# Performance work log

Hardware: AMD Instinct MI355X
Metric: run time of the kernel (lower is better)

## Reference

```python
import jax, jax.numpy as jnp
import numpy as np

EPS_RMS = 1e-6   # assumed eps for utils.rms
EPS_LN = 1e-5    # matches F.layer_norm eps in LayerNorm


def rmsnorm(z):
    # utils.rms: normalize to unit RMS over the channel dim
    return z * jax.lax.rsqrt(jnp.mean(jnp.square(z), axis=-1, keepdims=True) + EPS_RMS)


def layernorm(x, w):
    mu = jnp.mean(x, axis=-1, keepdims=True)
    var = jnp.var(x, axis=-1, keepdims=True)
    return (x - mu) * jax.lax.rsqrt(var + EPS_LN) * w


def polar_orthogonal(W):
    # utils.fast_polar_decomposition: orthogonal factor of polar decomposition
    U, _, Vh = jnp.linalg.svd(W, full_matrices=False)
    return U @ Vh


def pscan2(q, P1, P2, identity):
    # Hillis-Steele inclusive parallel scan over the time axis with combine
    # scan(left, right) = rms(left @ P1^T + right @ P2^T); positions with no
    # left operand at a level keep their current value (identity pads the shift).
    B, T, C = q.shape
    d = 1
    while d < T:
        left = jnp.concatenate(
            [jnp.broadcast_to(identity, (B, d, C)), q[:, : T - d]], axis=1)
        z = rmsnorm(jnp.einsum('btc,dc->btd', left, P1)
                    + jnp.einsum('btc,dc->btd', q, P2))
        upd = (jnp.arange(T) >= d)[None, :, None]
        q = jnp.where(upd, z, q)
        d *= 2
    return q


def setup_inputs() -> dict:
    key = jax.random.key(0)
    ks = jax.random.split(key, 9)
    B, T, C = 4, 4096, 512
    inv = 1.0 / np.sqrt(C)
    return {
        'x': jax.random.normal(ks[0], (B, T, C), jnp.float32),
        'ln1_w': jnp.ones((C,), jnp.float32),
        'Wq': jax.random.normal(ks[1], (C, C), jnp.float32) * inv,
        'Wv': jax.random.normal(ks[2], (C, C), jnp.float32) * inv,
        'Wo': jax.random.normal(ks[3], (C, C), jnp.float32) * inv,
        'identity': jax.random.uniform(ks[4], (C,), jnp.float32),
        'Wp1': jax.random.normal(ks[5], (C, C), jnp.float32),
        'Wp2': jax.random.normal(ks[6], (C, C), jnp.float32),
        'ln2_w': jnp.ones((C,), jnp.float32),
        'Wfc': jax.random.normal(ks[7], (4 * C, C), jnp.float32) * inv,
        'Wpr': jax.random.normal(ks[8], (C, 4 * C), jnp.float32) * (1.0 / np.sqrt(4 * C)),
    }


def reference(x, ln1_w, Wq, Wv, Wo, identity, Wp1, Wp2, ln2_w, Wfc, Wpr):
    # SSM branch (dropout = 0 in eval)
    h = layernorm(x, ln1_w)
    q = h @ Wq.T
    v = h @ Wv.T
    P1 = polar_orthogonal(Wp1)
    P2 = polar_orthogonal(Wp2)
    q = pscan2(q, P1, P2, identity)
    x = x + (q * v) @ Wo.T
    # MLP branch
    h2 = layernorm(x, ln2_w)
    h2 = jax.nn.gelu(h2 @ Wfc.T, approximate=False)  # torch nn.GELU() is exact erf
    x = x + h2 @ Wpr.T
    return x
```

## Files before the change

### kernel.cpp

```cpp
#include <hip/hip_runtime.h>
#include <hip/hip_bf16.h>

typedef __hip_bfloat16 bf16;
typedef __attribute__((ext_vector_type(8))) short short8;
typedef __attribute__((ext_vector_type(4))) short short4v;
typedef __attribute__((ext_vector_type(4))) float f32x4;

#define DEVINL static __device__ __forceinline__

DEVINL float b2f(bf16 x) { return __bfloat162float(x); }
DEVINL bf16 f2b(float x) { return __float2bfloat16(x); }
DEVINL float sb2f(short s) { return b2f(__builtin_bit_cast(bf16, s)); }
DEVINL short f2sb(float x) { return __builtin_bit_cast(short, f2b(x)); }

DEVINL void gload16(const void* g, void* l) {
  __builtin_amdgcn_global_load_lds(
      (const __attribute__((address_space(1))) void*)g,
      (__attribute__((address_space(3))) void*)l, 16, 0, 0);
}

DEVINL float wave_sum(float v) {
#pragma unroll
  for (int o = 32; o > 0; o >>= 1) v += __shfl_down(v, o, 64);
  return v;
}

DEVINL float wave_allsum(float v) {
#pragma unroll
  for (int o = 32; o > 0; o >>= 1) v += __shfl_xor(v, o, 64);
  return v;
}

DEVINL float gelu_exact(float v) {
  const float z = v * 0.70710678118654752f;
  const float az = fabsf(z);
  const float t = 1.0f / (1.0f + 0.3275911f * az);
  float p = 1.061405429f;
  p = p * t - 1.453152027f;
  p = p * t + 1.421413741f;
  p = p * t - 0.284496736f;
  p = p * t + 0.254829592f;
  const float e = __expf(-z * z);
  const float erf_az = 1.0f - p * t * e;
  const float er = (z < 0.f) ? -erf_az : erf_az;
  return 0.5f * v * (1.0f + er);
}

#define BARRIER()                             \
  do {                                        \
    __asm__ __volatile__("" ::: "memory");    \
    __builtin_amdgcn_s_barrier();             \
    __asm__ __volatile__("" ::: "memory");    \
  } while (0)
#define WAIT_LGKM0() __asm__ __volatile__("s_waitcnt lgkmcnt(0)" ::: "memory")
#define WAIT_VM(n) __asm__ __volatile__("s_waitcnt vmcnt(" #n ")" ::: "memory")

template <int MODE, bool SPLIT, int BM>
__global__ __launch_bounds__(256) void gemm_nt(
    const bf16* __restrict__ A0, const bf16* __restrict__ A1,
    const bf16* __restrict__ B0, const bf16* __restrict__ B1,
    int K, int lda, int ldb, long bsA, long bsB, long bsC,
    float alpha, float beta, float* __restrict__ Xf,
    bf16* __restrict__ Whi, bf16* __restrict__ Wlo,
    bf16* __restrict__ Thi, bf16* __restrict__ Tlo) {
  constexpr int BK = 64;
  constexpr int MT = BM / 32;
  constexpr int NLOAD = BM * BK / 2048;
  extern __shared__ char smem[];
  bf16* AsH = (bf16*)smem;
  bf16* BsH = AsH + BM * BK;
  bf16* AsL = BsH + BM * BK;
  bf16* BsL = AsL + BM * BK;

  const int t = threadIdx.x;
  const int lane = t & 63, w = t >> 6;
  const long bz = blockIdx.z;
  const bf16* Ab0 = A0 + bz * bsA;
  const bf16* Bb0 = B0 + bz * bsB;
  const bf16* Ab1 = SPLIT ? (A1 + bz * bsA) : nullptr;
  const bf16* Bb1 = SPLIT ? (B1 + bz * bsB) : nullptr;

  const int row0 = blockIdx.x * BM, col0 = blockIdx.y * BM;
  const int wm = (w >> 1) * (BM / 2), wn = (w & 1) * (BM / 2);
  const int jj = lane >> 4, r16 = lane & 15;

  f32x4 acc[MT][MT] = {};

  for (int k0 = 0; k0 < K; k0 += BK) {
    __syncthreads();
#pragma unroll
    for (int s = 0; s < NLOAD; ++s) {
      const int L = s * 256 + t;
      const int cj = L / BM, m = L % BM;
      const long ga = (long)(row0 + m) * lda + (k0 + cj * 8);
      const long gb = (long)(col0 + m) * ldb + (k0 + cj * 8);
      gload16(Ab0 + ga, AsH + L * 8);
      gload16(Bb0 + gb, BsH + L * 8);
      if (SPLIT) {
        gload16(Ab1 + ga, AsL + L * 8);
        gload16(Bb1 + gb, BsL + L * 8);
      }
    }
    __syncthreads();

#pragma unroll
    for (int kk = 0; kk < BK / 32; ++kk) {
      short8 a[MT], b[MT], al[MT], bl[MT];
#pragma unroll
      for (int mt = 0; mt < MT; ++mt) {
        const int o = (kk * 4 + jj) * BM * 8 + (wm + mt * 16 + r16) * 8;
        a[mt] = *(const short8*)(AsH + o);
        if (SPLIT) al[mt] = *(const short8*)(AsL + o);
      }
#pragma unroll
      for (int nt = 0; nt < MT; ++nt) {
        const int o = (kk * 4 + jj) * BM * 8 + (wn + nt * 16 + r16) * 8;
        b[nt] = *(const short8*)(BsH + o);
        if (SPLIT) bl[nt] = *(const short8*)(BsL + o);
      }
#pragma unroll
      for (int mt = 0; mt < MT; ++mt)
#pragma unroll
        for (int nt = 0; nt < MT; ++nt) {
          acc[mt][nt] = __builtin_amdgcn_mfma_f32_16x16x32_bf16(a[mt], b[nt], acc[mt][nt], 0, 0, 0);
          if (SPLIT) {
            acc[mt][nt] = __builtin_amdgcn_mfma_f32_16x16x32_bf16(a[mt], bl[nt], acc[mt][nt], 0, 0, 0);
            acc[mt][nt] = __builtin_amdgcn_mfma_f32_16x16x32_bf16(al[mt], b[nt], acc[mt][nt], 0, 0, 0);
          }
        }
    }
  }

#pragma unroll
  for (int mt = 0; mt < MT; ++mt)
#pragma unroll
    for (int nt = 0; nt < MT; ++nt)
#pragma unroll
      for (int r = 0; r < 4; ++r) {
        const int row = row0 + wm + mt * 16 + jj * 4 + r;
        const int col = col0 + wn + nt * 16 + r16;
        const float v = acc[mt][nt][r];
        if (MODE == 3) {
          const long i = bz * bsC + (long)row * 512 + col;
          const bf16 h = f2b(v);
          Whi[i] = h;
          Wlo[i] = f2b(v - b2f(h));
        } else if (MODE == 4) {
          const long i = bz * bsC + (long)row * 512 + col;
          const float nv = alpha * Xf[i] + beta * v;
          Xf[i] = nv;
          const bf16 h = f2b(nv);
          const bf16 l = f2b(nv - b2f(h));
          Whi[i] = h; Wlo[i] = l;
          const long it2 = bz * bsC + (long)col * 512 + row;
          Thi[it2] = h; Tlo[it2] = l;
        }
      }
}

DEVINL void loadA4(const bf16* p, short8 (&dst)[4][2]) {
#pragma unroll
  for (int mf = 0; mf < 4; ++mf)
#pragma unroll
    for (int kk = 0; kk < 2; ++kk)
      dst[mf][kk] = *(const short8*)(p + kk * 4096 + mf * 128);
}
DEVINL void loadB2(const bf16* p, short8 (&dst)[2][2]) {
#pragma unroll
  for (int nf = 0; nf < 2; ++nf)
#pragma unroll
    for (int kk = 0; kk < 2; ++kk)
      dst[nf][kk] = *(const short8*)(p + kk * 4096 + nf * 128);
}
template <int QM, int QN>
DEVINL void mfma16(const short8 (&af)[4][2], const short8 (&bb)[2][2],
                   f32x4 (&acc)[8][4]) {
  __builtin_amdgcn_s_setprio(1);
#pragma unroll
  for (int mf = 0; mf < 4; ++mf)
#pragma unroll
    for (int nf = 0; nf < 2; ++nf)
#pragma unroll
      for (int kk = 0; kk < 2; ++kk)
        acc[QM * 4 + mf][QN * 2 + nf] = __builtin_amdgcn_mfma_f32_16x16x32_bf16(
            af[mf][kk], bb[nf][kk], acc[QM * 4 + mf][QN * 2 + nf], 0, 0, 0);
  __builtin_amdgcn_s_setprio(0);
}
template <int QM>
DEVINL void mfma16h(const short8 (&af)[4][2], const short8 (&bb)[2][2],
                    f32x4 (&acc)[8][2]) {
  __builtin_amdgcn_s_setprio(1);
#pragma unroll
  for (int mf = 0; mf < 4; ++mf)
#pragma unroll
    for (int nf = 0; nf < 2; ++nf)
#pragma unroll
      for (int kk = 0; kk < 2; ++kk)
        acc[QM * 4 + mf][nf] = __builtin_amdgcn_mfma_f32_16x16x32_bf16(
            af[mf][kk], bb[nf][kk], acc[QM * 4 + mf][nf], 0, 0, 0);
  __builtin_amdgcn_s_setprio(0);
}

template <int MODE, int BN>
__global__ __launch_bounds__(512, 2) void gemm256(
    const bf16* __restrict__ A, const bf16* __restrict__ B, int K, int lda,
    int ldb, bf16* __restrict__ outb, int ldo, const float* __restrict__ resf,
    float* __restrict__ outf) {
  extern __shared__ char smem[];
  const int t = threadIdx.x;
  const int lane = t & 63;
  const int w = t >> 6, wr = w >> 2, wc = w & 3;
  const int jj = lane >> 4, r16 = lane & 15;
  const int sm = t & 127, cj = t >> 7;

  int bx, by;
  {
    const int gx = gridDim.x;
    const int nwg = gx * gridDim.y;
    int lin = blockIdx.y * gx + blockIdx.x;
    lin = (lin & 7) * (nwg >> 3) + (lin >> 3);
    bx = lin % gx;
    by = lin / gx;
  }
  const int row0 = bx * 256;
  const int col0 = by * BN;

  const int aBase = (jj * 128 + wr * 64 + r16) * 8;
  const int bBase = (jj * 128 + wc * 32 + r16) * 8;

  if constexpr (BN == 256) {
    auto slotp = [&](int buf, int mat, int half) -> bf16* {
      return (bf16*)(smem + (((buf << 2) | (mat << 1) | half) << 14));
    };
    auto stageA = [&](int buf, int half, int kt) {
      bf16* dst = slotp(buf, 0, half) + t * 8;
      const long ga = (long)(row0 + half * 128 + sm) * lda + kt * 64 + cj * 8;
      gload16(A + ga, dst);
      gload16(A + ga + 32, dst + 4096);
    };
    auto stageB = [&](int buf, int half, int kt) {
      bf16* dst = slotp(buf, 1, half) + t * 8;
      const long gb = (long)(col0 + half * 128 + sm) * ldb + kt * 64 + cj * 8;
      gload16(B + gb, dst);
      gload16(B + gb + 32, dst + 4096);
    };

    f32x4 acc[8][4] = {};
    const int nit = K >> 7;

    stageA(0, 0, 0); stageB(0, 0, 0);
    stageB(0, 1, 0);
    stageA(0, 1, 0);
    stageA(1, 0, 1); stageB(1, 0, 1);
    stageB(1, 1, 1);
    WAIT_VM(8);
    BARRIER();

    for (int it = 0; it < nit; ++it) {
      const int k1 = 2 * it + 1, k2 = 2 * it + 2, k3 = 2 * it + 3;
      const bool more = (it + 1 < nit);
      short8 af[4][2], b0[2][2], b1[2][2];
      loadA4(slotp(0, 0, 0) + aBase, af);
      loadB2(slotp(0, 1, 0) + bBase, b0);
      stageA(1, 1, k1);
      BARRIER(); WAIT_LGKM0();
      mfma16<0, 0>(af, b0, acc);
      loadB2(slotp(0, 1, 1) + bBase, b1);
      WAIT_VM(8);
      BARRIER(); WAIT_LGKM0();
      mfma16<0, 1>(af, b1, acc);
      loadA4(slotp(0, 0, 1) + aBase, af);
      if (more) { stageA(0, 0, k2); stageB(0, 0, k2); }
      BARRIER(); WAIT_LGKM0();
      mfma16<1, 1>(af, b1, acc);
      if (more) { stageB(0, 1, k2); WAIT_VM(8); } else { WAIT_VM(0); }
      BARRIER();
      mfma16<1, 0>(af, b0, acc);
      loadA4(slotp(1, 0, 0) + aBase, af);
      loadB2(slotp(1, 1, 0) + bBase, b0);
      if (more) stageA(0, 1, k2);
      BARRIER(); WAIT_LGKM0();
      mfma16<0, 0>(af, b0, acc);
      loadB2(slotp(1, 1, 1) + bBase, b1);
      WAIT_VM(8);
      BARRIER(); WAIT_LGKM0();
      mfma16<0, 1>(af, b1, acc);
      loadA4(slotp(1, 0, 1) + aBase, af);
      if (more) { stageA(1, 0, k3); stageB(1, 0, k3); }
      BARRIER(); WAIT_LGKM0();
      mfma16<1, 1>(af, b1, acc);
      if (more) { stageB(1, 1, k3); WAIT_VM(8); }
      BARRIER();
      mfma16<1, 0>(af, b0, acc);
    }

    if constexpr (MODE == 2) {
#pragma unroll
      for (int q = 0; q < 8; ++q)
#pragma unroll
        for (int n = 0; n < 4; ++n)
#pragma unroll
          for (int r = 0; r < 4; ++r) {
            const int row = row0 + (q >> 2) * 128 + wr * 64 + (q & 3) * 16 + jj * 4 + r;
            const int col = col0 + (n >> 1) * 128 + wc * 32 + (n & 1) * 16 + r16;
            const long i = (long)row * ldo + col;
            outf[i] = resf[i] + acc[q][n][r];
          }
      return;
    } else {
      __syncthreads();
      bf16* Cs = (bf16*)smem;
#pragma unroll
      for (int q = 0; q < 8; ++q)
#pragma unroll
        for (int n = 0; n < 4; ++n)
#pragma unroll
          for (int r = 0; r < 4; ++r) {
            const int row = (q >> 2) * 128 + wr * 64 + (q & 3) * 16 + jj * 4 + r;
            const int col = (n >> 1) * 128 + wc * 32 + (n & 1) * 16 + r16;
            float v = acc[q][n][r];
            if (MODE == 1) v = gelu_exact(v);
            Cs[row * 256 + col] = f2b(v);
          }
      __syncthreads();
#pragma unroll
      for (int i = 0; i < 16; ++i) {
        const int rr = i * 16 + (t >> 5);
        const int cc = (t & 31) * 8;
        *(short8*)(outb + (long)(row0 + rr) * ldo + (col0 + cc)) =
            *(const short8*)(Cs + rr * 256 + cc);
      }
    }
  } else {
    auto slotp3 = [&](int buf, int slot) -> bf16* {
      return (bf16*)(smem + ((buf * 3 + slot) << 14));
    };
    auto stage3A = [&](int buf, int half, int kt) {
      bf16* dst = slotp3(buf, half) + t * 8;
      const long ga = (long)(row0 + half * 128 + sm) * lda + kt * 64 + cj * 8;
      gload16(A + ga, dst);
      gload16(A + ga + 32, dst + 4096);
    };
    auto stage3B = [&](int buf, int kt) {
      bf16* dst = slotp3(buf, 2) + t * 8;
      const long gb = (long)(col0 + sm) * ldb + kt * 64 + cj * 8;
      gload16(B + gb, dst);
      gload16(B + gb + 32, dst + 4096);
    };

    f32x4 acc[8][2] = {};
    const int nt = K >> 6;

    stage3A(0, 0, 0); stage3A(0, 1, 0); stage3B(0, 0);
    stage3A(1, 0, 1); stage3A(1, 1, 1); stage3B(1, 1);
    WAIT_VM(6);
    BARRIER();

    int cb = 0;
    for (int tk = 0; tk < nt; ++tk) {
      int sb = cb + 2; if (sb >= 3) sb -= 3;
      const bool more = (tk + 2 < nt);
      short8 af[4][2], bb2[2][2];
      bf16* sA0 = slotp3(cb, 0);
      bf16* sA1 = slotp3(cb, 1);
      bf16* sB = slotp3(cb, 2);
      loadA4(sA0 + aBase, af);
      loadB2(sB + bBase, bb2);
      if (more) { stage3A(sb, 0, tk + 2); stage3B(sb, tk + 2); }
      BARRIER(); WAIT_LGKM0();
      mfma16h<0>(af, bb2, acc);
      loadA4(sA1 + aBase, af);
      if (more) stage3A(sb, 1, tk + 2);
      if (more) { WAIT_VM(6); } else { WAIT_VM(0); }
      BARRIER(); WAIT_LGKM0();
      mfma16h<1>(af, bb2, acc);
      cb = (cb + 1 == 3) ? 0 : cb + 1;
    }

#pragma unroll
    for (int q = 0; q < 8; ++q)
#pragma unroll
      for (int n = 0; n < 2; ++n)
#pragma unroll
        for (int r = 0; r < 4; ++r) {
          const int row = row0 + (q >> 2) * 128 + wr * 64 + (q & 3) * 16 + jj * 4 + r;
          const int col = col0 + wc * 32 + n * 16 + r16;
          const long i = (long)row * ldo + col;
          outf[i] = resf[i] + acc[q][n][r];
        }
  }
}

__global__ __launch_bounds__(256) void fnorm(const float* __restrict__ W1,
                                             const float* __restrict__ W2,
                                             float* __restrict__ sigsq) {
  const int b = blockIdx.x >> 8;
  const float4 v = *(const float4*)((b ? W2 : W1) +
                                    (((long)(blockIdx.x & 255) * 256 + threadIdx.x) << 2));
  float s = v.x * v.x + v.y * v.y + v.z * v.z + v.w * v.w;
  s = wave_sum(s);
  if ((threadIdx.x & 63) == 0) atomicAdd(&sigsq[b], s);
}

__global__ __launch_bounds__(256) void scale_init(
    const float* __restrict__ W1, const float* __restrict__ W2,
    const float* __restrict__ sigsq, float* __restrict__ Xf,
    bf16* __restrict__ Xhi, bf16* __restrict__ Xlo,
    bf16* __restrict__ Thi, bf16* __restrict__ Tlo) {
  const long idx = (long)blockIdx.x * 256 + threadIdx.x;
  const int b = (int)(idx >> 18);
  const int i = (int)(idx & 262143);
  const float s = rsqrtf(sigsq[b]);
  const float val = (b ? W2[i] : W1[i]) * s;
  const long o = ((long)b << 18) + i;
  Xf[o] = val;
  const bf16 h = f2b(val);
  const bf16 l = f2b(val - b2f(h));
  Xhi[o] = h; Xlo[o] = l;
  const int r = i >> 9, c = i & 511;
  const long ot = ((long)b << 18) + (long)c * 512 + r;
  Thi[ot] = h; Tlo[ot] = l;
}

__global__ __launch_bounds__(256) void convert_weights(
    const float* __restrict__ Wq, const float* __restrict__ Wv,
    const float* __restrict__ Wo, const float* __restrict__ Wfc,
    const float* __restrict__ Wpr, bf16* __restrict__ Wqvb,
    bf16* __restrict__ Wob, bf16* __restrict__ Wfcb, bf16* __restrict__ Wprb) {
  const long e = ((long)blockIdx.x * 256 + threadIdx.x) << 2;
  const float* src; bf16* dst; long off;
  if (e < 262144)       { src = Wq;  dst = Wqvb;          off = e; }
  else if (e < 524288)  { src = Wv;  dst = Wqvb + 262144; off = e - 262144; }
  else if (e < 786432)  { src = Wo;  dst = Wob;           off = e - 524288; }
  else if (e < 1835008) { src = Wfc; dst = Wfcb;          off = e - 786432; }
  else                  { src = Wpr; dst = Wprb;          off = e - 1835008; }
  const float4 v = *(const float4*)(src + off);
  short4v o4;
  o4[0] = f2sb(v.x); o4[1] = f2sb(v.y); o4[2] = f2sb(v.z); o4[3] = f2sb(v.w);
  *(short4v*)(dst + off) = o4;
}

__global__ __launch_bounds__(256) void ln_rows(const float* __restrict__ x,
                                               const float* __restrict__ w,
                                               bf16* __restrict__ out) {
  const int row = (blockIdx.x << 2) + (threadIdx.x >> 6);
  const int lane = threadIdx.x & 63;
  const float* xr = x + (long)row * 512 + lane * 8;
  const float4 a = *(const float4*)xr;
  const float4 b = *(const float4*)(xr + 4);
  float v[8] = {a.x, a.y, a.z, a.w, b.x, b.y, b.z, b.w};
  float s1 = 0.f, s2 = 0.f;
#pragma unroll
  for (int i = 0; i < 8; ++i) { s1 += v[i]; s2 += v[i] * v[i]; }
  s1 = wave_allsum(s1);
  s2 = wave_allsum(s2);
  const float mean = s1 * (1.0f / 512.0f);
  const float var = s2 * (1.0f / 512.0f) - mean * mean;
  const float inv = rsqrtf(var + 1e-5f);
  const float4 w1 = *(const float4*)(w + lane * 8);
  const float4 w2 = *(const float4*)(w + lane * 8 + 4);
  const float wv[8] = {w1.x, w1.y, w1.z, w1.w, w2.x, w2.y, w2.z, w2.w};
  short8 o8;
#pragma unroll
  for (int i = 0; i < 8; ++i) o8[i] = f2sb((v[i] - mean) * inv * wv[i]);
  *(short8*)(out + (long)row * 512 + lane * 8) = o8;
}

__global__ __launch_bounds__(256) void pscan_combine2(const bf16* __restrict__ Y,
                                                      bf16* __restrict__ QV, int d) {
  const int span = 4096 - d;
  const int wid = (blockIdx.x << 2) + (threadIdx.x >> 6);
  const int lane = threadIdx.x & 63;
  const int b = wid / span;
  const int tt = d + (wid - b * span);
  const long row2 = (long)b * 4096 + tt;
  const long row1 = row2 - d;
  const short8 a8 = *(const short8*)(Y + row1 * 1024 + lane * 8);
  const short8 b8 = *(const short8*)(Y + row2 * 1024 + 512 + lane * 8);
  float s[8]; float ss = 0.f;
#pragma unroll
  for (int i = 0; i < 8; ++i) {
    const float v = sb2f(a8[i]) + sb2f(b8[i]);
    s[i] = v; ss += v * v;
  }
  ss = wave_allsum(ss);
  const float inv = rsqrtf(ss * (1.0f / 512.0f) + 1e-6f);
  short8 o8;
#pragma unroll
  for (int i = 0; i < 8; ++i) o8[i] = f2sb(s[i] * inv);
  *(short8*)(QV + row2 * 1024 + lane * 8) = o8;
}

__global__ __launch_bounds__(256) void qv_mul(const bf16* __restrict__ QV,
                                              bf16* __restrict__ u) {
  const long base = ((long)blockIdx.x * 256 + threadIdx.x) << 3;
  const long row = base >> 9;
  const int c = (int)(base & 511);
  const short8 q8 = *(const short8*)(QV + row * 1024 + c);
  const short8 v8 = *(const short8*)(QV + row * 1024 + 512 + c);
  short8 o8;
#pragma unroll
  for (int i = 0; i < 8; ++i) o8[i] = f2sb(sb2f(q8[i]) * sb2f(v8[i]));
  *(short8*)(u + row * 512 + c) = o8;
}

extern "C" void kernel_launch(void* const* d_in, const int* in_sizes, int n_in,
                              void* d_out, int out_size, void* d_ws, size_t ws_size,
                              hipStream_t stream) {
  (void)in_sizes; (void)n_in; (void)out_size; (void)ws_size;
  const float* x    = (const float*)d_in[0];
  const float* ln1w = (const float*)d_in[1];
  const float* Wq   = (const float*)d_in[2];
  const float* Wv   = (const float*)d_in[3];
  const float* Wo   = (const float*)d_in[4];
  const float* Wp1  = (const float*)d_in[6];
  const float* Wp2  = (const float*)d_in[7];
  const float* ln2w = (const float*)d_in[8];
  const float* Wfc  = (const float*)d_in[9];
  const float* Wpr  = (const float*)d_in[10];
  float* out = (float*)d_out;

  const long M = 16384;
  char* ws = (char*)d_ws;
  size_t off = 0;
  auto alloc = [&](size_t bytes) -> void* {
    void* p = ws + off;
    off += (bytes + 255) & ~(size_t)255;
    return p;
  };
  bf16* YZ   = (bf16*)alloc(M * 1024 * 2);
  bf16* QV   = (bf16*)alloc(M * 1024 * 2);
  bf16* hb   = (bf16*)alloc(M * 512 * 2);
  bf16* Wqvb = (bf16*)alloc(1024 * 512 * 2);
  bf16* Wob  = (bf16*)alloc(512 * 512 * 2);
  bf16* Wfcb = (bf16*)alloc(2048 * 512 * 2);
  bf16* Wprb = (bf16*)alloc(512 * 2048 * 2);
  float* Xf  = (float*)alloc(2 * 262144 * 4);
  bf16* Xhi  = (bf16*)alloc(2 * 262144 * 2);
  bf16* Xlo  = (bf16*)alloc(2 * 262144 * 2);
  bf16* XtAh = (bf16*)alloc(2 * 262144 * 2);
  bf16* XtAl = (bf16*)alloc(2 * 262144 * 2);
  bf16* XtBh = (bf16*)alloc(2 * 262144 * 2);
  bf16* XtBl = (bf16*)alloc(2 * 262144 * 2);
  bf16* Ghi  = (bf16*)alloc(2 * 262144 * 2);
  bf16* Glo  = (bf16*)alloc(2 * 262144 * 2);
  float* sig = (float*)alloc(256);
  bf16* Y  = YZ;
  bf16* h3 = YZ;

  const auto Z0 = nullptr;

  hipMemsetAsync(sig, 0, 2 * sizeof(float), stream);
  fnorm<<<512, 256, 0, stream>>>(Wp1, Wp2, sig);
  scale_init<<<2048, 256, 0, stream>>>(Wp1, Wp2, sig, Xf, Xhi, Xlo, XtAh, XtAl);

  bf16 *tch = XtAh, *tcl = XtAl, *tnh = XtBh, *tnl = XtBl;
  const long Sz = 262144;
  for (int i = 0; i < 20; ++i) {
    const bool pol = (i >= 16);
    const float ac = pol ? 1.5f : 2.0f;
    const float bc = pol ? -0.5f : -1.0f;
    dim3 g(8, 8, 2);
    gemm_nt<3, true, 64><<<g, 256, 32768, stream>>>(
        Xhi, Xlo, Xhi, Xlo, 512, 512, 512, Sz, Sz, Sz,
        0.f, 0.f, Z0, Ghi, Glo, Z0, Z0);
    gemm_nt<4, true, 64><<<g, 256, 32768, stream>>>(
        Ghi, Glo, tch, tcl, 512, 512, 512, Sz, Sz, Sz,
        ac, bc, Xf, Xhi, Xlo, tnh, tnl);
    bf16* sw;
    sw = tch; tch = tnh; tnh = sw;
    sw = tcl; tcl = tnl; tnl = sw;
  }

  convert_weights<<<2816, 256, 0, stream>>>(Wq, Wv, Wo, Wfc, Wpr, Wqvb, Wob, Wfcb, Wprb);

  ln_rows<<<4096, 256, 0, stream>>>(x, ln1w, hb);
  gemm256<0, 256><<<dim3(64, 4), 512, 131072, stream>>>(
      hb, Wqvb, 512, 512, 512, QV, 1024, Z0, Z0);

  for (int d = 1; d < 4096; d <<= 1) {
    gemm256<0, 256><<<dim3(64, 4), 512, 131072, stream>>>(
        QV, Xhi, 512, 1024, 512, Y, 1024, Z0, Z0);
    pscan_combine2<<<4096 - d, 256, 0, stream>>>(Y, QV, d);
  }

  qv_mul<<<4096, 256, 0, stream>>>(QV, hb);
  gemm256<2, 128><<<dim3(64, 4), 512, 147456, stream>>>(
      hb, Wob, 512, 512, 512, Z0, 512, x, out);

  ln_rows<<<4096, 256, 0, stream>>>(out, ln2w, hb);
  gemm256<1, 256><<<dim3(64, 8), 512, 131072, stream>>>(
      hb, Wfcb, 512, 512, 512, h3, 2048, Z0, Z0);
  gemm256<2, 128><<<dim3(64, 4), 512, 147456, stream>>>(
      h3, Wprb, 2048, 2048, 2048, Z0, 512, out, out);
}
```

Before: 1.466 ms.

## Fuse pscan shifted operands into one K=1024 GEMM and skip finished rows

Each pscan level now runs a single GEMM whose A operand concatenates the d-shifted left row with the current row along K (K=1024), against a repacked [P1|P2] weight. This removes the separate add of two halves of a 1024-wide output. The grid covers only row tiles from d rounded down to 256, so already-final prefix rows are skipped at later levels. The BN=128 path gains a bf16 LDS-staged epilogue and reorders its prefetch issue. The costs are a 2x deeper K per tile, clamped addressing for shifted rows, and the swizzled block mapping being dropped for all GEMMs.

```diff
diff --git a/kernel.cpp b/kernel.cpp
--- a/kernel.cpp
+++ b/kernel.cpp
@@ -201,11 +201,11 @@
   __builtin_amdgcn_s_setprio(0);
 }
 
-template <int MODE, int BN>
+template <int MODE, int BN, bool PSCAN>
 __global__ __launch_bounds__(512, 2) void gemm256(
     const bf16* __restrict__ A, const bf16* __restrict__ B, int K, int lda,
     int ldb, bf16* __restrict__ outb, int ldo, const float* __restrict__ resf,
-    float* __restrict__ outf) {
+    float* __restrict__ outf, int d, int start, int nyb) {
   extern __shared__ char smem[];
   const int t = threadIdx.x;
   const int lane = t & 63;
@@ -213,17 +213,16 @@
   const int jj = lane >> 4, r16 = lane & 15;
   const int sm = t & 127, cj = t >> 7;
 
-  int bx, by;
-  {
-    const int gx = gridDim.x;
-    const int nwg = gx * gridDim.y;
-    int lin = blockIdx.y * gx + blockIdx.x;
-    lin = (lin & 7) * (nwg >> 3) + (lin >> 3);
-    bx = lin % gx;
-    by = lin / gx;
+  int row0, batch0 = 0;
+  if (PSCAN) {
+    const int b = blockIdx.x / nyb;
+    const int ty = blockIdx.x - b * nyb;
+    batch0 = b * 4096;
+    row0 = batch0 + start + ty * 256;
+  } else {
+    row0 = blockIdx.x * 256;
   }
-  const int row0 = bx * 256;
-  const int col0 = by * BN;
+  const int col0 = blockIdx.y * BN;
 
   const int aBase = (jj * 128 + wr * 64 + r16) * 8;
   const int bBase = (jj * 128 + wc * 32 + r16) * 8;
@@ -337,7 +336,19 @@
     };
     auto stage3A = [&](int buf, int half, int kt) {
       bf16* dst = slotp3(buf, half) + t * 8;
-      const long ga = (long)(row0 + half * 128 + sm) * lda + kt * 64 + cj * 8;
+      long ga;
+      if (PSCAN) {
+        const int rr = row0 + half * 128 + sm;
+        if (kt < 8) {
+          int rs = rr - d;
+          if (rs < batch0) rs = batch0;
+          ga = (long)rs * 1024 + kt * 64 + cj * 8;
+        } else {
+          ga = (long)rr * 1024 + (kt - 8) * 64 + cj * 8;
+        }
+      } else {
+        ga = (long)(row0 + half * 128 + sm) * lda + kt * 64 + cj * 8;
+      }
       gload16(A + ga, dst);
       gload16(A + ga + 32, dst + 4096);
     };
@@ -366,29 +377,64 @@
       bf16* sB = slotp3(cb, 2);
       loadA4(sA0 + aBase, af);
       loadB2(sB + bBase, bb2);
-      if (more) { stage3A(sb, 0, tk + 2); stage3B(sb, tk + 2); }
       BARRIER(); WAIT_LGKM0();
       mfma16h<0>(af, bb2, acc);
       loadA4(sA1 + aBase, af);
-      if (more) stage3A(sb, 1, tk + 2);
-      if (more) { WAIT_VM(6); } else { WAIT_VM(0); }
+      if (more) {
+        stage3A(sb, 0, tk + 2); stage3A(sb, 1, tk + 2); stage3B(sb, tk + 2);
+        WAIT_VM(6);
+      } else {
+        WAIT_VM(0);
+      }
       BARRIER(); WAIT_LGKM0();
       mfma16h<1>(af, bb2, acc);
       cb = (cb + 1 == 3) ? 0 : cb + 1;
     }
 
-#pragma unroll
-    for (int q = 0; q < 8; ++q)
-#pragma unroll
-      for (int n = 0; n < 2; ++n)
-#pragma unroll
-        for (int r = 0; r < 4; ++r) {
-          const int row = row0 + (q >> 2) * 128 + wr * 64 + (q & 3) * 16 + jj * 4 + r;
-          const int col = col0 + wc * 32 + n * 16 + r16;
-          const long i = (long)row * ldo + col;
-          outf[i] = resf[i] + acc[q][n][r];
-        }
+    if constexpr (MODE == 2) {
+#pragma unroll
+      for (int q = 0; q < 8; ++q)
+#pragma unroll
+        for (int n = 0; n < 2; ++n)
+#pragma unroll
+          for (int r = 0; r < 4; ++r) {
+            const int row = row0 + (q >> 2) * 128 + wr * 64 + (q & 3) * 16 + jj * 4 + r;
+            const int col = col0 + wc * 32 + n * 16 + r16;
+            const long i = (long)row * ldo + col;
+            outf[i] = resf[i] + acc[q][n][r];
+          }
+    } else {
+      __syncthreads();
+      bf16* Cs = (bf16*)smem;
+#pragma unroll
+      for (int q = 0; q < 8; ++q)
+#pragma unroll
+        for (int n = 0; n < 2; ++n)
+#pragma unroll
+          for (int r = 0; r < 4; ++r) {
+            const int row = (q >> 2) * 128 + wr * 64 + (q & 3) * 16 + jj * 4 + r;
+            const int col = wc * 32 + n * 16 + r16;
+            Cs[row * 128 + col] = f2b(acc[q][n][r]);
+          }
+      __syncthreads();
+#pragma unroll
+      for (int i = 0; i < 8; ++i) {
+        const int rr = i * 32 + (t >> 4);
+        const int cc = (t & 15) * 8;
+        *(short8*)(outb + (long)(row0 + rr) * ldo + (col0 + cc)) =
+            *(const short8*)(Cs + rr * 128 + cc);
+      }
+    }
   }
+}
+
+__global__ __launch_bounds__(256) void repack_pcat(const bf16* __restrict__ Xhi,
+                                                   bf16* __restrict__ Pcat) {
+  const int e = (blockIdx.x * 256 + threadIdx.x) << 3;
+  const int c = e >> 10, k = e & 1023;
+  const bf16* src = (k < 512) ? (Xhi + (long)c * 512 + k)
+                              : (Xhi + 262144 + (long)c * 512 + (k - 512));
+  *(short8*)(Pcat + e) = *(const short8*)src;
 }
 
 __global__ __launch_bounds__(256) void fnorm(const float* __restrict__ W1,
@@ -466,21 +512,19 @@
   *(short8*)(out + (long)row * 512 + lane * 8) = o8;
 }
 
-__global__ __launch_bounds__(256) void pscan_combine2(const bf16* __restrict__ Y,
-                                                      bf16* __restrict__ QV, int d) {
+__global__ __launch_bounds__(256) void pscan_combine(const bf16* __restrict__ S,
+                                                     bf16* __restrict__ QV, int d) {
   const int span = 4096 - d;
   const int wid = (blockIdx.x << 2) + (threadIdx.x >> 6);
   const int lane = threadIdx.x & 63;
   const int b = wid / span;
   const int tt = d + (wid - b * span);
-  const long row2 = (long)b * 4096 + tt;
-  const long row1 = row2 - d;
-  const short8 a8 = *(const short8*)(Y + row1 * 1024 + lane * 8);
-  const short8 b8 = *(const short8*)(Y + row2 * 1024 + 512 + lane * 8);
+  const long rowQ = (long)b * 4096 + tt;
+  const short8 s8 = *(const short8*)(S + rowQ * 512 + lane * 8);
   float s[8]; float ss = 0.f;
 #pragma unroll
   for (int i = 0; i < 8; ++i) {
-    const float v = sb2f(a8[i]) + sb2f(b8[i]);
+    const float v = sb2f(s8[i]);
     s[i] = v; ss += v * v;
   }
   ss = wave_allsum(ss);
@@ -488,7 +532,7 @@
   short8 o8;
 #pragma unroll
   for (int i = 0; i < 8; ++i) o8[i] = f2sb(s[i] * inv);
-  *(short8*)(QV + row2 * 1024 + lane * 8) = o8;
+  *(short8*)(QV + rowQ * 1024 + lane * 8) = o8;
 }
 
 __global__ __launch_bounds__(256) void qv_mul(const bf16* __restrict__ QV,
@@ -544,8 +588,9 @@
   bf16* XtBl = (bf16*)alloc(2 * 262144 * 2);
   bf16* Ghi  = (bf16*)alloc(2 * 262144 * 2);
   bf16* Glo  = (bf16*)alloc(2 * 262144 * 2);
+  bf16* Pcat = (bf16*)alloc(512 * 1024 * 2);
   float* sig = (float*)alloc(256);
-  bf16* Y  = YZ;
+  bf16* S  = YZ;
   bf16* h3 = YZ;
 
   const auto Z0 = nullptr;
@@ -571,26 +616,29 @@
     sw = tch; tch = tnh; tnh = sw;
     sw = tcl; tcl = tnl; tnl = sw;
   }
+  repack_pcat<<<256, 256, 0, stream>>>(Xhi, Pcat);
 
   convert_weights<<<2816, 256, 0, stream>>>(Wq, Wv, Wo, Wfc, Wpr, Wqvb, Wob, Wfcb, Wprb);
 
   ln_rows<<<4096, 256, 0, stream>>>(x, ln1w, hb);
-  gemm256<0, 256><<<dim3(64, 4), 512, 131072, stream>>>(
-      hb, Wqvb, 512, 512, 512, QV, 1024, Z0, Z0);
+  gemm256<0, 256, false><<<dim3(64, 4), 512, 131072, stream>>>(
+      hb, Wqvb, 512, 512, 512, QV, 1024, Z0, Z0, 0, 0, 0);
 
   for (int d = 1; d < 4096; d <<= 1) {
-    gemm256<0, 256><<<dim3(64, 4), 512, 131072, stream>>>(
-        QV, Xhi, 512, 1024, 512, Y, 1024, Z0, Z0);
-    pscan_combine2<<<4096 - d, 256, 0, stream>>>(Y, QV, d);
+    const int start = d & ~255;
+    const int nyb = (4096 - start) >> 8;
+    gemm256<0, 128, true><<<dim3(4 * nyb, 4), 512, 147456, stream>>>(
+        QV, Pcat, 1024, 1024, 1024, S, 512, Z0, Z0, d, start, nyb);
+    pscan_combine<<<4096 - d, 256, 0, stream>>>(S, QV, d);
   }
 
   qv_mul<<<4096, 256, 0, stream>>>(QV, hb);
-  gemm256<2, 128><<<dim3(64, 4), 512, 147456, stream>>>(
-      hb, Wob, 512, 512, 512, Z0, 512, x, out);
+  gemm256<2, 128, false><<<dim3(64, 4), 512, 147456, stream>>>(
+      hb, Wob, 512, 512, 512, Z0, 512, x, out, 0, 0, 0);
 
   ln_rows<<<4096, 256, 0, stream>>>(out, ln2w, hb);
-  gemm256<1, 256><<<dim3(64, 8), 512, 131072, stream>>>(
-      hb, Wfcb, 512, 512, 512, h3, 2048, Z0, Z0);
-  gemm256<2, 128><<<dim3(64, 4), 512, 147456, stream>>>(
-      h3, Wprb, 2048, 2048, 2048, Z0, 512, out, out);
-}
+  gemm256<1, 256, false><<<dim3(64, 8), 512, 131072, stream>>>(
+      hb, Wfcb, 512, 512, 512, h3, 2048, Z0, Z0, 0, 0, 0);
+  gemm256<2, 128, false><<<dim3(64, 4), 512, 147456, stream>>>(
+      h3, Wprb, 2048, 2048, 2048, Z0, 512, out, out, 0, 0, 0);
+}
```

Measured after the change: 1.498 ms. +2.2%, slower.

## Fuse parallel-scan GEMM with RMS-norm combine into one kernel per level

Applied to the files above, without the earlier changes.

Replaces the per-level pair of a GEMM (q against both polar factors into a 1024-wide Y) plus a separate combine kernel with a single kernel. It computes [q_shifted, q] @ [P1;P2]^T over K=1024, RMS-normalises in registers/LDS, and writes the new q directly, ping-ponging between two buffers. It also repacks P1/P2 into a concatenated matrix, removes the block-swizzle from gemm256, and moves all prefetch issues of gemm256 after the first MFMA half. The goal is to avoid the Y round-trip through memory and one launch per level. The tradeoff is a 64-row tile with only 256 blocks at one block per CU, each re-reading the full 1 MB weight.

```diff
diff --git a/kernel.cpp b/kernel.cpp
--- a/kernel.cpp
+++ b/kernel.cpp
@@ -213,17 +213,8 @@
   const int jj = lane >> 4, r16 = lane & 15;
   const int sm = t & 127, cj = t >> 7;
 
-  int bx, by;
-  {
-    const int gx = gridDim.x;
-    const int nwg = gx * gridDim.y;
-    int lin = blockIdx.y * gx + blockIdx.x;
-    lin = (lin & 7) * (nwg >> 3) + (lin >> 3);
-    bx = lin % gx;
-    by = lin / gx;
-  }
-  const int row0 = bx * 256;
-  const int col0 = by * BN;
+  const int row0 = blockIdx.x * 256;
+  const int col0 = blockIdx.y * BN;
 
   const int aBase = (jj * 128 + wr * 64 + r16) * 8;
   const int bBase = (jj * 128 + wc * 32 + r16) * 8;
@@ -366,12 +357,15 @@
       bf16* sB = slotp3(cb, 2);
       loadA4(sA0 + aBase, af);
       loadB2(sB + bBase, bb2);
-      if (more) { stage3A(sb, 0, tk + 2); stage3B(sb, tk + 2); }
       BARRIER(); WAIT_LGKM0();
       mfma16h<0>(af, bb2, acc);
       loadA4(sA1 + aBase, af);
-      if (more) stage3A(sb, 1, tk + 2);
-      if (more) { WAIT_VM(6); } else { WAIT_VM(0); }
+      if (more) {
+        stage3A(sb, 0, tk + 2); stage3A(sb, 1, tk + 2); stage3B(sb, tk + 2);
+        WAIT_VM(6);
+      } else {
+        WAIT_VM(0);
+      }
       BARRIER(); WAIT_LGKM0();
       mfma16h<1>(af, bb2, acc);
       cb = (cb + 1 == 3) ? 0 : cb + 1;
@@ -389,6 +383,144 @@
           outf[i] = resf[i] + acc[q][n][r];
         }
   }
+}
+
+__global__ __launch_bounds__(512, 1) void pscan_fused(
+    const bf16* __restrict__ Qsrc, int ldq, bf16* __restrict__ Qdst,
+    const bf16* __restrict__ Pcat, int d) {
+  extern __shared__ char smem[];
+  __shared__ float sums[64][4];
+  const int t = threadIdx.x;
+  const int lane = t & 63;
+  const int w = t >> 6, wr = w >> 2, wc = w & 3;
+  const int jj = lane >> 4, r16 = lane & 15;
+
+  const int b = blockIdx.x >> 6;
+  const int ty = blockIdx.x & 63;
+  const int batch0 = b * 4096;
+  const int row0 = batch0 + ty * 64;
+
+  auto Asp = [&](int buf) -> bf16* { return (bf16*)smem + buf * 4096; };
+  auto Bsp = [&](int buf) -> bf16* { return (bf16*)(smem + 16384) + buf * 32768; };
+
+  bf16* Cs = (bf16*)smem;
+
+  if (row0 - batch0 + 63 >= d) {
+    const int am = t & 63, acj = t >> 6;
+    auto stage = [&](int kt, int buf) {
+      {
+        long ga;
+        const int rr = row0 + am;
+        if (kt < 8) {
+          int rs = rr - d;
+          if (rs < batch0) rs = batch0;
+          ga = (long)rs * ldq + kt * 64 + acj * 8;
+        } else {
+          ga = (long)rr * ldq + (kt - 8) * 64 + acj * 8;
+        }
+        gload16(Qsrc + ga, Asp(buf) + t * 8);
+      }
+      bf16* bs = Bsp(buf);
+#pragma unroll
+      for (int s = 0; s < 8; ++s)
+        gload16(Pcat + (long)t * 1024 + kt * 64 + s * 8, bs + (s * 512 + t) * 8);
+    };
+
+    f32x4 acc[2][8] = {};
+    stage(0, 0);
+    WAIT_VM(0);
+    BARRIER();
+
+    int cur = 0;
+    for (int kt = 0; kt < 16; ++kt) {
+      if (kt < 15) stage(kt + 1, cur ^ 1);
+      const bf16* as = Asp(cur);
+      const bf16* bs = Bsp(cur);
+#pragma unroll
+      for (int kk = 0; kk < 2; ++kk) {
+        short8 a[2], bb[8];
+#pragma unroll
+        for (int mt = 0; mt < 2; ++mt)
+          a[mt] = *(const short8*)(as + ((kk * 4 + jj) * 64 + wr * 32 + mt * 16 + r16) * 8);
+#pragma unroll
+        for (int nt = 0; nt < 8; ++nt)
+          bb[nt] = *(const short8*)(bs + ((kk * 4 + jj) * 512 + wc * 128 + nt * 16 + r16) * 8);
+#pragma unroll
+        for (int mt = 0; mt < 2; ++mt)
+#pragma unroll
+          for (int nt = 0; nt < 8; ++nt)
+            acc[mt][nt] = __builtin_amdgcn_mfma_f32_16x16x32_bf16(
+                a[mt], bb[nt], acc[mt][nt], 0, 0, 0);
+      }
+      if (kt < 15) WAIT_VM(0);
+      WAIT_LGKM0();
+      BARRIER();
+      cur ^= 1;
+    }
+
+    float part[2][4];
+#pragma unroll
+    for (int mt = 0; mt < 2; ++mt)
+#pragma unroll
+      for (int r = 0; r < 4; ++r) {
+        float s = 0.f;
+#pragma unroll
+        for (int nt = 0; nt < 8; ++nt) {
+          const float v = acc[mt][nt][r];
+          s += v * v;
+        }
+        part[mt][r] = s;
+      }
+#pragma unroll
+    for (int off = 1; off < 16; off <<= 1)
+#pragma unroll
+      for (int mt = 0; mt < 2; ++mt)
+#pragma unroll
+        for (int r = 0; r < 4; ++r)
+          part[mt][r] += __shfl_xor(part[mt][r], off, 64);
+    if (r16 == 0) {
+#pragma unroll
+      for (int mt = 0; mt < 2; ++mt)
+#pragma unroll
+        for (int r = 0; r < 4; ++r)
+          sums[wr * 32 + mt * 16 + jj * 4 + r][wc] = part[mt][r];
+    }
+    __syncthreads();
+#pragma unroll
+    for (int mt = 0; mt < 2; ++mt)
+#pragma unroll
+      for (int r = 0; r < 4; ++r) {
+        const int rl = wr * 32 + mt * 16 + jj * 4 + r;
+        const float tot = sums[rl][0] + sums[rl][1] + sums[rl][2] + sums[rl][3];
+        const float inv = rsqrtf(tot * (1.0f / 512.0f) + 1e-6f);
+#pragma unroll
+        for (int nt = 0; nt < 8; ++nt)
+          Cs[rl * 512 + wc * 128 + nt * 16 + r16] = f2b(acc[mt][nt][r] * inv);
+      }
+    __syncthreads();
+  }
+
+#pragma unroll
+  for (int s = 0; s < 8; ++s) {
+    const int j = s * 512 + t;
+    const int rl = j >> 6, c8 = (j & 63) * 8;
+    const int trel = row0 + rl - batch0;
+    short8 v8;
+    if (trel >= d)
+      v8 = *(const short8*)(Cs + rl * 512 + c8);
+    else
+      v8 = *(const short8*)(Qsrc + (long)(row0 + rl) * ldq + c8);
+    *(short8*)(Qdst + (long)(row0 + rl) * 512 + c8) = v8;
+  }
+}
+
+__global__ __launch_bounds__(256) void repack_pcat(const bf16* __restrict__ Xhi,
+                                                   bf16* __restrict__ Pcat) {
+  const int e = (blockIdx.x * 256 + threadIdx.x) << 3;
+  const int c = e >> 10, k = e & 1023;
+  const bf16* src = (k < 512) ? (Xhi + (long)c * 512 + k)
+                              : (Xhi + 262144 + (long)c * 512 + (k - 512));
+  *(short8*)(Pcat + e) = *(const short8*)src;
 }
 
 __global__ __launch_bounds__(256) void fnorm(const float* __restrict__ W1,
@@ -466,37 +598,13 @@
   *(short8*)(out + (long)row * 512 + lane * 8) = o8;
 }
 
-__global__ __launch_bounds__(256) void pscan_combine2(const bf16* __restrict__ Y,
-                                                      bf16* __restrict__ QV, int d) {
-  const int span = 4096 - d;
-  const int wid = (blockIdx.x << 2) + (threadIdx.x >> 6);
-  const int lane = threadIdx.x & 63;
-  const int b = wid / span;
-  const int tt = d + (wid - b * span);
-  const long row2 = (long)b * 4096 + tt;
-  const long row1 = row2 - d;
-  const short8 a8 = *(const short8*)(Y + row1 * 1024 + lane * 8);
-  const short8 b8 = *(const short8*)(Y + row2 * 1024 + 512 + lane * 8);
-  float s[8]; float ss = 0.f;
-#pragma unroll
-  for (int i = 0; i < 8; ++i) {
-    const float v = sb2f(a8[i]) + sb2f(b8[i]);
-    s[i] = v; ss += v * v;
-  }
-  ss = wave_allsum(ss);
-  const float inv = rsqrtf(ss * (1.0f / 512.0f) + 1e-6f);
-  short8 o8;
-#pragma unroll
-  for (int i = 0; i < 8; ++i) o8[i] = f2sb(s[i] * inv);
-  *(short8*)(QV + row2 * 1024 + lane * 8) = o8;
-}
-
-__global__ __launch_bounds__(256) void qv_mul(const bf16* __restrict__ QV,
+__global__ __launch_bounds__(256) void qv_mul(const bf16* __restrict__ Q,
+                                              const bf16* __restrict__ QV,
                                               bf16* __restrict__ u) {
   const long base = ((long)blockIdx.x * 256 + threadIdx.x) << 3;
   const long row = base >> 9;
   const int c = (int)(base & 511);
-  const short8 q8 = *(const short8*)(QV + row * 1024 + c);
+  const short8 q8 = *(const short8*)(Q + row * 512 + c);
   const short8 v8 = *(const short8*)(QV + row * 1024 + 512 + c);
   short8 o8;
 #pragma unroll
@@ -544,8 +652,10 @@
   bf16* XtBl = (bf16*)alloc(2 * 262144 * 2);
   bf16* Ghi  = (bf16*)alloc(2 * 262144 * 2);
   bf16* Glo  = (bf16*)alloc(2 * 262144 * 2);
+  bf16* Pcat = (bf16*)alloc(512 * 1024 * 2);
   float* sig = (float*)alloc(256);
-  bf16* Y  = YZ;
+  bf16* Qa = YZ;
+  bf16* Qb = YZ + 8388608;
   bf16* h3 = YZ;
 
   const auto Z0 = nullptr;
@@ -571,6 +681,7 @@
     sw = tch; tch = tnh; tnh = sw;
     sw = tcl; tcl = tnl; tnl = sw;
   }
+  repack_pcat<<<256, 256, 0, stream>>>(Xhi, Pcat);
 
   convert_weights<<<2816, 256, 0, stream>>>(Wq, Wv, Wo, Wfc, Wpr, Wqvb, Wob, Wfcb, Wprb);
 
@@ -578,13 +689,19 @@
   gemm256<0, 256><<<dim3(64, 4), 512, 131072, stream>>>(
       hb, Wqvb, 512, 512, 512, QV, 1024, Z0, Z0);
 
-  for (int d = 1; d < 4096; d <<= 1) {
-    gemm256<0, 256><<<dim3(64, 4), 512, 131072, stream>>>(
-        QV, Xhi, 512, 1024, 512, Y, 1024, Z0, Z0);
-    pscan_combine2<<<4096 - d, 256, 0, stream>>>(Y, QV, d);
+  {
+    const bf16* qsrc = QV;
+    int ldq = 1024;
+    bf16* qdst = Qa;
+    for (int d = 1; d < 4096; d <<= 1) {
+      pscan_fused<<<256, 512, 147456, stream>>>(qsrc, ldq, qdst, Pcat, d);
+      qsrc = qdst;
+      ldq = 512;
+      qdst = (qdst == Qa) ? Qb : Qa;
+    }
+    qv_mul<<<4096, 256, 0, stream>>>(qsrc, QV, hb);
   }
 
-  qv_mul<<<4096, 256, 0, stream>>>(QV, hb);
   gemm256<2, 128><<<dim3(64, 4), 512, 147456, stream>>>(
       hb, Wob, 512, 512, 512, Z0, 512, x, out);
 
```

Measured after the change: 1.667 ms. 1.14x slower.

## Pipeline Newton-Schulz split-bf16 GEMM with triple-buffered async LDS staging

Applied to the files above, without the earlier changes.

Replaces the generic single-buffered gemm_nt used in the 20 polar-decomposition iterations with a specialised gemm_ns. It has fixed K=512, triple-buffered LDS, and prefetches two tiles ahead via global_load_lds, so loads overlap the MFMA work on hi/lo splits. It also removes the XCD-style block remapping in gemm256 and moves the prefetch issue in gemm256 after the first MFMA half, which changes memory locality and overlap. The cost is three times the LDS per block (96KB), which may reduce occupancy.

```diff
diff --git a/kernel.cpp b/kernel.cpp
--- a/kernel.cpp
+++ b/kernel.cpp
@@ -55,86 +55,109 @@
 #define WAIT_LGKM0() __asm__ __volatile__("s_waitcnt lgkmcnt(0)" ::: "memory")
 #define WAIT_VM(n) __asm__ __volatile__("s_waitcnt vmcnt(" #n ")" ::: "memory")
 
-template <int MODE, bool SPLIT, int BM>
-__global__ __launch_bounds__(256) void gemm_nt(
+template <int MODE>
+__global__ __launch_bounds__(256) void gemm_ns(
     const bf16* __restrict__ A0, const bf16* __restrict__ A1,
     const bf16* __restrict__ B0, const bf16* __restrict__ B1,
-    int K, int lda, int ldb, long bsA, long bsB, long bsC,
+    long bsA, long bsB, long bsC,
     float alpha, float beta, float* __restrict__ Xf,
     bf16* __restrict__ Whi, bf16* __restrict__ Wlo,
     bf16* __restrict__ Thi, bf16* __restrict__ Tlo) {
-  constexpr int BK = 64;
-  constexpr int MT = BM / 32;
-  constexpr int NLOAD = BM * BK / 2048;
   extern __shared__ char smem[];
-  bf16* AsH = (bf16*)smem;
-  bf16* BsH = AsH + BM * BK;
-  bf16* AsL = BsH + BM * BK;
-  bf16* BsL = AsL + BM * BK;
-
   const int t = threadIdx.x;
   const int lane = t & 63, w = t >> 6;
   const long bz = blockIdx.z;
   const bf16* Ab0 = A0 + bz * bsA;
   const bf16* Bb0 = B0 + bz * bsB;
-  const bf16* Ab1 = SPLIT ? (A1 + bz * bsA) : nullptr;
-  const bf16* Bb1 = SPLIT ? (B1 + bz * bsB) : nullptr;
-
-  const int row0 = blockIdx.x * BM, col0 = blockIdx.y * BM;
-  const int wm = (w >> 1) * (BM / 2), wn = (w & 1) * (BM / 2);
+  const bf16* Ab1 = A1 + bz * bsA;
+  const bf16* Bb1 = B1 + bz * bsB;
+  const int row0 = blockIdx.x * 64, col0 = blockIdx.y * 64;
+  const int wm = (w >> 1) * 32, wn = (w & 1) * 32;
   const int jj = lane >> 4, r16 = lane & 15;
 
-  f32x4 acc[MT][MT] = {};
-
-  for (int k0 = 0; k0 < K; k0 += BK) {
-    __syncthreads();
-#pragma unroll
-    for (int s = 0; s < NLOAD; ++s) {
+  auto buf = [&](int b, int arr) -> bf16* {
+    return (bf16*)(smem + b * 32768 + arr * 8192);
+  };
+  auto stage = [&](int bi, int kt) {
+#pragma unroll
+    for (int s = 0; s < 2; ++s) {
       const int L = s * 256 + t;
-      const int cj = L / BM, m = L % BM;
-      const long ga = (long)(row0 + m) * lda + (k0 + cj * 8);
-      const long gb = (long)(col0 + m) * ldb + (k0 + cj * 8);
-      gload16(Ab0 + ga, AsH + L * 8);
-      gload16(Bb0 + gb, BsH + L * 8);
-      if (SPLIT) {
-        gload16(Ab1 + ga, AsL + L * 8);
-        gload16(Bb1 + gb, BsL + L * 8);
+      const int cj = L >> 6, m = L & 63;
+      const long ga = (long)(row0 + m) * 512 + kt * 64 + cj * 8;
+      const long gb = (long)(col0 + m) * 512 + kt * 64 + cj * 8;
+      gload16(Ab0 + ga, buf(bi, 0) + L * 8);
+      gload16(Bb0 + gb, buf(bi, 1) + L * 8);
+      gload16(Ab1 + ga, buf(bi, 2) + L * 8);
+      gload16(Bb1 + gb, buf(bi, 3) + L * 8);
+    }
+  };
+
+  f32x4 acc[2][2] = {};
+
+  stage(0, 0); stage(1, 1);
+  WAIT_VM(8);
+  BARRIER();
+
+  for (int tk = 0; tk < 8; ++tk) {
+    const int cb = tk % 3;
+    const int sb = (tk + 2) % 3;
+    bf16* ah = buf(cb, 0); bf16* bh = buf(cb, 1);
+    bf16* alp = buf(cb, 2); bf16* blp = buf(cb, 3);
+    short8 a[2], b[2], al[2], bl[2];
+#pragma unroll
+    for (int mt = 0; mt < 2; ++mt) {
+      const int o = (jj * 64 + wm + mt * 16 + r16) * 8;
+      a[mt] = *(const short8*)(ah + o);
+      al[mt] = *(const short8*)(alp + o);
+    }
+#pragma unroll
+    for (int nt = 0; nt < 2; ++nt) {
+      const int o = (jj * 64 + wn + nt * 16 + r16) * 8;
+      b[nt] = *(const short8*)(bh + o);
+      bl[nt] = *(const short8*)(blp + o);
+    }
+    BARRIER(); WAIT_LGKM0();
+#pragma unroll
+    for (int mt = 0; mt < 2; ++mt)
+#pragma unroll
+      for (int nt = 0; nt < 2; ++nt) {
+        acc[mt][nt] = __builtin_amdgcn_mfma_f32_16x16x32_bf16(a[mt], b[nt], acc[mt][nt], 0, 0, 0);
+        acc[mt][nt] = __builtin_amdgcn_mfma_f32_16x16x32_bf16(a[mt], bl[nt], acc[mt][nt], 0, 0, 0);
+        acc[mt][nt] = __builtin_amdgcn_mfma_f32_16x16x32_bf16(al[mt], b[nt], acc[mt][nt], 0, 0, 0);
       }
-    }
-    __syncthreads();
-
-#pragma unroll
-    for (int kk = 0; kk < BK / 32; ++kk) {
-      short8 a[MT], b[MT], al[MT], bl[MT];
-#pragma unroll
-      for (int mt = 0; mt < MT; ++mt) {
-        const int o = (kk * 4 + jj) * BM * 8 + (wm + mt * 16 + r16) * 8;
-        a[mt] = *(const short8*)(AsH + o);
-        if (SPLIT) al[mt] = *(const short8*)(AsL + o);
+#pragma unroll
+    for (int mt = 0; mt < 2; ++mt) {
+      const int o = ((4 + jj) * 64 + wm + mt * 16 + r16) * 8;
+      a[mt] = *(const short8*)(ah + o);
+      al[mt] = *(const short8*)(alp + o);
+    }
+#pragma unroll
+    for (int nt = 0; nt < 2; ++nt) {
+      const int o = ((4 + jj) * 64 + wn + nt * 16 + r16) * 8;
+      b[nt] = *(const short8*)(bh + o);
+      bl[nt] = *(const short8*)(blp + o);
+    }
+    if (tk + 2 < 8) {
+      stage(sb, tk + 2);
+      WAIT_VM(8);
+    } else if (tk + 1 < 8) {
+      WAIT_VM(0);
+    }
+    BARRIER(); WAIT_LGKM0();
+#pragma unroll
+    for (int mt = 0; mt < 2; ++mt)
+#pragma unroll
+      for (int nt = 0; nt < 2; ++nt) {
+        acc[mt][nt] = __builtin_amdgcn_mfma_f32_16x16x32_bf16(a[mt], b[nt], acc[mt][nt], 0, 0, 0);
+        acc[mt][nt] = __builtin_amdgcn_mfma_f32_16x16x32_bf16(a[mt], bl[nt], acc[mt][nt], 0, 0, 0);
+        acc[mt][nt] = __builtin_amdgcn_mfma_f32_16x16x32_bf16(al[mt], b[nt], acc[mt][nt], 0, 0, 0);
       }
-#pragma unroll
-      for (int nt = 0; nt < MT; ++nt) {
-        const int o = (kk * 4 + jj) * BM * 8 + (wn + nt * 16 + r16) * 8;
-        b[nt] = *(const short8*)(BsH + o);
-        if (SPLIT) bl[nt] = *(const short8*)(BsL + o);
-      }
-#pragma unroll
-      for (int mt = 0; mt < MT; ++mt)
-#pragma unroll
-        for (int nt = 0; nt < MT; ++nt) {
-          acc[mt][nt] = __builtin_amdgcn_mfma_f32_16x16x32_bf16(a[mt], b[nt], acc[mt][nt], 0, 0, 0);
-          if (SPLIT) {
-            acc[mt][nt] = __builtin_amdgcn_mfma_f32_16x16x32_bf16(a[mt], bl[nt], acc[mt][nt], 0, 0, 0);
-            acc[mt][nt] = __builtin_amdgcn_mfma_f32_16x16x32_bf16(al[mt], b[nt], acc[mt][nt], 0, 0, 0);
-          }
-        }
-    }
   }
 
 #pragma unroll
-  for (int mt = 0; mt < MT; ++mt)
-#pragma unroll
-    for (int nt = 0; nt < MT; ++nt)
+  for (int mt = 0; mt < 2; ++mt)
+#pragma unroll
+    for (int nt = 0; nt < 2; ++nt)
 #pragma unroll
       for (int r = 0; r < 4; ++r) {
         const int row = row0 + wm + mt * 16 + jj * 4 + r;
@@ -145,7 +168,7 @@
           const bf16 h = f2b(v);
           Whi[i] = h;
           Wlo[i] = f2b(v - b2f(h));
-        } else if (MODE == 4) {
+        } else {
           const long i = bz * bsC + (long)row * 512 + col;
           const float nv = alpha * Xf[i] + beta * v;
           Xf[i] = nv;
@@ -213,17 +236,8 @@
   const int jj = lane >> 4, r16 = lane & 15;
   const int sm = t & 127, cj = t >> 7;
 
-  int bx, by;
-  {
-    const int gx = gridDim.x;
-    const int nwg = gx * gridDim.y;
-    int lin = blockIdx.y * gx + blockIdx.x;
-    lin = (lin & 7) * (nwg >> 3) + (lin >> 3);
-    bx = lin % gx;
-    by = lin / gx;
-  }
-  const int row0 = bx * 256;
-  const int col0 = by * BN;
+  const int row0 = blockIdx.x * 256;
+  const int col0 = blockIdx.y * BN;
 
   const int aBase = (jj * 128 + wr * 64 + r16) * 8;
   const int bBase = (jj * 128 + wc * 32 + r16) * 8;
@@ -366,12 +380,15 @@
       bf16* sB = slotp3(cb, 2);
       loadA4(sA0 + aBase, af);
       loadB2(sB + bBase, bb2);
-      if (more) { stage3A(sb, 0, tk + 2); stage3B(sb, tk + 2); }
       BARRIER(); WAIT_LGKM0();
       mfma16h<0>(af, bb2, acc);
       loadA4(sA1 + aBase, af);
-      if (more) stage3A(sb, 1, tk + 2);
-      if (more) { WAIT_VM(6); } else { WAIT_VM(0); }
+      if (more) {
+        stage3A(sb, 0, tk + 2); stage3A(sb, 1, tk + 2); stage3B(sb, tk + 2);
+        WAIT_VM(6);
+      } else {
+        WAIT_VM(0);
+      }
       BARRIER(); WAIT_LGKM0();
       mfma16h<1>(af, bb2, acc);
       cb = (cb + 1 == 3) ? 0 : cb + 1;
@@ -561,12 +578,10 @@
     const float ac = pol ? 1.5f : 2.0f;
     const float bc = pol ? -0.5f : -1.0f;
     dim3 g(8, 8, 2);
-    gemm_nt<3, true, 64><<<g, 256, 32768, stream>>>(
-        Xhi, Xlo, Xhi, Xlo, 512, 512, 512, Sz, Sz, Sz,
-        0.f, 0.f, Z0, Ghi, Glo, Z0, Z0);
-    gemm_nt<4, true, 64><<<g, 256, 32768, stream>>>(
-        Ghi, Glo, tch, tcl, 512, 512, 512, Sz, Sz, Sz,
-        ac, bc, Xf, Xhi, Xlo, tnh, tnl);
+    gemm_ns<3><<<g, 256, 98304, stream>>>(
+        Xhi, Xlo, Xhi, Xlo, Sz, Sz, Sz, 0.f, 0.f, Z0, Ghi, Glo, Z0, Z0);
+    gemm_ns<4><<<g, 256, 98304, stream>>>(
+        Ghi, Glo, tch, tcl, Sz, Sz, Sz, ac, bc, Xf, Xhi, Xlo, tnh, tnl);
     bf16* sw;
     sw = tch; tch = tnh; tnh = sw;
     sw = tcl; tcl = tnl; tnl = sw;
```

Result: faster. 1.294 ms (-11.8%).
